# Kernel optimization log

Measured on AMD Instinct MI355X. Metric: run time of the kernel, lower is better.

The kernel has to match this reference:

```python
import jax, jax.numpy as jnp
import numpy as np

N = 131072
H = 64
CMB_RADIUS_KM = 3485.0


def setup_inputs() -> dict:
    key = jax.random.key(0)
    ks = jax.random.split(key, 8)
    phi = jax.random.uniform(ks[0], (N, 1), jnp.float32, 0.0, 2.0 * np.pi)
    # keep theta away from the poles so sin(theta) != 0
    theta = jax.random.uniform(ks[1], (N, 1), jnp.float32, 0.1, np.pi - 0.1)
    radius = jnp.full((N, 1), CMB_RADIUS_KM, dtype=jnp.float32)
    horiz_theta = jax.random.normal(ks[2], (N, 1), jnp.float32) * 0.01
    horiz_phi = jax.random.normal(ks[3], (N, 1), jnp.float32) * 0.01
    br = jax.random.normal(ks[4], (N, 1), jnp.float32) * 100.0
    W1 = jax.random.normal(ks[5], (2, H), jnp.float32) / np.sqrt(2.0)
    b1 = jnp.zeros((H,), jnp.float32)
    W2 = jax.random.normal(ks[6], (H, H), jnp.float32) / np.sqrt(H)
    b2 = jnp.zeros((H,), jnp.float32)
    W3 = jax.random.normal(ks[7], (H, 1), jnp.float32) / np.sqrt(H)
    b3 = jnp.zeros((1,), jnp.float32)
    return dict(phi=phi, theta=theta, radius=radius, horiz_theta=horiz_theta,
                horiz_phi=horiz_phi, br=br, W1=W1, b1=b1, W2=W2, b2=b2, W3=W3, b3=b3)


def reference(phi, theta, radius, horiz_theta, horiz_phi, br, W1, b1, W2, b2, W3, b3):
    sin = jnp.sin

    # per-point scalar network; input order matches torch.cat([phi, theta], dim=1)
    def T(p, t):
        x = jnp.stack([p, t])
        h = jnp.tanh(x @ W1 + b1)
        h = jnp.tanh(h @ W2 + b2)
        return (h @ W3 + b3)[0]

    dTp = jax.grad(T, 0)
    dTt = jax.grad(T, 1)

    # In the torch code T = model(X) and P = model(X) are the same function,
    # so T_x == P_x and the flows simplify to:
    def u_th(p, t):
        return dTp(p, t) / sin(t) + dTt(p, t)

    def u_ph(p, t):
        return dTp(p, t) / sin(t) - dTt(p, t)

    # nested derivatives exactly as the chained autograd.grad calls
    u_th_t = jax.grad(lambda p, t: -u_th(p, t) * sin(t), 1)            # u_theta_theta
    u_th_tt = jax.grad(lambda p, t: u_th_t(p, t) * sin(t), 1)          # u_theta_theta_theta
    u_th_p = jax.grad(lambda p, t: -u_th(p, t), 0)                     # u_theta_phi
    u_th_pp = jax.grad(u_th_p, 0)                                      # u_theta_phi_phi
    u_ph_t = jax.grad(lambda p, t: u_ph(p, t) * sin(t), 1)             # u_phi_theta
    u_ph_tt = jax.grad(lambda p, t: u_ph_t(p, t) * sin(t), 1)          # u_phi_theta_theta
    u_ph_p = jax.grad(u_ph, 0)                                         # u_phi_phi
    u_ph_pp = jax.grad(u_ph_p, 0)                                      # u_phi_phi_phi

    def per_point(p, t):
        return (u_th(p, t), u_ph(p, t), u_th_t(p, t), u_th_tt(p, t),
                u_th_pp(p, t), u_ph_tt(p, t), u_ph_p(p, t), u_ph_pp(p, t))

    vals = jax.vmap(per_point)(phi.ravel(), theta.ravel())
    ut, up, utt, uttt, utpp, uphtt, upp, uppp = [v.reshape(-1, 1) for v in vals]

    s = sin(theta)
    div_uh = (utt + upp) / (radius * s)
    u_theta_lap = s / radius ** 2 * uttt + utpp / (radius * s) ** 2
    u_phi_lap = s / radius ** 2 * uphtt + uppp / (radius * s) ** 2
    comp = s * (u_theta_lap ** 2 + u_phi_lap ** 2)
    sv_out = -(ut * horiz_theta + up * horiz_phi) - br * div_uh
    tg_con = div_uh - ut * jnp.tan(theta) / radius
    return (ut, up, div_uh, sv_out, tg_con, comp)
```

## Files before the change

kernel.cpp:

```cpp
#include <hip/hip_runtime.h>

#define NH 64

typedef _Float16 half8 __attribute__((ext_vector_type(8)));
typedef float float4v __attribute__((ext_vector_type(4)));

__device__ __forceinline__ float fast_tanh(float x) {
  float e = __expf(2.0f * x);
  float r = __builtin_amdgcn_rcpf(e + 1.0f);
  return fmaf(-2.0f, r, 1.0f);
}

__global__ __launch_bounds__(256) __attribute__((amdgpu_waves_per_eu(2, 2)))
void pinn_mfma(
    const float* __restrict__ phi, const float* __restrict__ theta,
    const float* __restrict__ radius, const float* __restrict__ hth,
    const float* __restrict__ hph, const float* __restrict__ br,
    const float* __restrict__ W1, const float* __restrict__ b1,
    const float* __restrict__ W2, const float* __restrict__ b2,
    const float* __restrict__ W3, float* __restrict__ out, int n) {
  __shared__ _Float16 Bs[2 * 4096];

  for (int i = threadIdx.x; i < 4096; i += 256) {
    int h = i >> 6, j = i & 63;
    float w2 = W2[i];
    int nt = j >> 4, cl = j & 15, ks = h >> 5, q = (h >> 3) & 3, j2 = h & 7;
    int base = (nt * 2 + ks) * 512 + (q * 16 + cl) * 8 + j2;
    _Float16 hi = (_Float16)w2;
    Bs[base] = hi;
    Bs[base + 4096] = (_Float16)(w2 - (float)hi);
  }
  __syncthreads();

  const int lane = threadIdx.x & 63;
  const int wave = threadIdx.x >> 6;
  const int tile = blockIdx.x * 4 + wave;
  const int quad = lane >> 4, col = lane & 15;
  const int pbase = tile * 16;
  if (pbase >= n) return;

  float p = phi[pbase + col], t = theta[pbase + col];
  half8 A0h[2], A0l[2], A1h[2], A1l[2], A2h[2], A2l[2];
  half8 A3[2], A4[2], A5[2], A6[2], A7[2], A8[2], A9[2];
#pragma unroll
  for (int ks = 0; ks < 2; ++ks) {
#pragma unroll
    for (int jj = 0; jj < 8; ++jj) {
      int h = ks * 32 + quad * 8 + jj;
      float a = W1[h], b = W1[NH + h];
      float z = fmaf(p, a, fmaf(t, b, b1[h]));
      float y = fast_tanh(z);
      float f1 = fmaf(-y, y, 1.0f);
      float f3 = f1 * fmaf(-6.0f, f1, 4.0f);
      float na = -2.0f * (y * f1);
      float a2 = a * a, ab = a * b, bb = b * b;
      float f3a2 = f3 * a2, f3bb = f3 * bb;
      float v1 = f1 * a, v2 = f1 * b;
      _Float16 yh = (_Float16)y;
      _Float16 v1h = (_Float16)v1;
      _Float16 v2h = (_Float16)v2;
      A0h[ks][jj] = yh;   A0l[ks][jj] = (_Float16)(y - (float)yh);
      A1h[ks][jj] = v1h;  A1l[ks][jj] = (_Float16)(v1 - (float)v1h);
      A2h[ks][jj] = v2h;  A2l[ks][jj] = (_Float16)(v2 - (float)v2h);
      A3[ks][jj] = (_Float16)(na * a2);
      A4[ks][jj] = (_Float16)(na * ab);
      A5[ks][jj] = (_Float16)(na * bb);
      A6[ks][jj] = (_Float16)(f3a2 * a);
      A7[ks][jj] = (_Float16)(f3a2 * b);
      A8[ks][jj] = (_Float16)(f3bb * a);
      A9[ks][jj] = (_Float16)(f3bb * b);
    }
  }

  const int rsel = col >> 2;
  const int pi = pbase + quad * 4 + rsel;
  float t2 = theta[pi];
  float rv = radius[pi];
  float hthv = hth[pi], hphv = hph[pi], brv = br[pi];
  float b2a[4], w3a[4];
#pragma unroll
  for (int nt = 0; nt < 4; ++nt) {
    b2a[nt] = b2[nt * 16 + col];
    w3a[nt] = W3[nt * 16 + col];
  }

  float4v Tacc[9];
#pragma unroll
  for (int x = 0; x < 9; ++x) Tacc[x] = (float4v){0.f, 0.f, 0.f, 0.f};

#pragma unroll
  for (int nt = 0; nt < 4; ++nt) {
    float4v acc[10];
#pragma unroll
    for (int k = 0; k < 10; ++k) acc[k] = (float4v){0.f, 0.f, 0.f, 0.f};
#pragma unroll
    for (int ks = 0; ks < 2; ++ks) {
      half8 bh = *(const half8*)(Bs + (nt * 2 + ks) * 512 + lane * 8);
      half8 bl = *(const half8*)(Bs + 4096 + (nt * 2 + ks) * 512 + lane * 8);
      acc[0] = __builtin_amdgcn_mfma_f32_16x16x32_f16(A0h[ks], bh, acc[0], 0, 0, 0);
      acc[0] = __builtin_amdgcn_mfma_f32_16x16x32_f16(A0l[ks], bh, acc[0], 0, 0, 0);
      acc[0] = __builtin_amdgcn_mfma_f32_16x16x32_f16(A0h[ks], bl, acc[0], 0, 0, 0);
      acc[1] = __builtin_amdgcn_mfma_f32_16x16x32_f16(A1h[ks], bh, acc[1], 0, 0, 0);
      acc[1] = __builtin_amdgcn_mfma_f32_16x16x32_f16(A1l[ks], bh, acc[1], 0, 0, 0);
      acc[1] = __builtin_amdgcn_mfma_f32_16x16x32_f16(A1h[ks], bl, acc[1], 0, 0, 0);
      acc[2] = __builtin_amdgcn_mfma_f32_16x16x32_f16(A2h[ks], bh, acc[2], 0, 0, 0);
      acc[2] = __builtin_amdgcn_mfma_f32_16x16x32_f16(A2l[ks], bh, acc[2], 0, 0, 0);
      acc[2] = __builtin_amdgcn_mfma_f32_16x16x32_f16(A2h[ks], bl, acc[2], 0, 0, 0);
      acc[3] = __builtin_amdgcn_mfma_f32_16x16x32_f16(A3[ks], bh, acc[3], 0, 0, 0);
      acc[4] = __builtin_amdgcn_mfma_f32_16x16x32_f16(A4[ks], bh, acc[4], 0, 0, 0);
      acc[5] = __builtin_amdgcn_mfma_f32_16x16x32_f16(A5[ks], bh, acc[5], 0, 0, 0);
      acc[6] = __builtin_amdgcn_mfma_f32_16x16x32_f16(A6[ks], bh, acc[6], 0, 0, 0);
      acc[7] = __builtin_amdgcn_mfma_f32_16x16x32_f16(A7[ks], bh, acc[7], 0, 0, 0);
      acc[8] = __builtin_amdgcn_mfma_f32_16x16x32_f16(A8[ks], bh, acc[8], 0, 0, 0);
      acc[9] = __builtin_amdgcn_mfma_f32_16x16x32_f16(A9[ks], bh, acc[9], 0, 0, 0);
    }
    float b2v = b2a[nt];
    float w3v = w3a[nt];
#pragma unroll
    for (int r = 0; r < 4; ++r) {
      float z0 = acc[0][r] + b2v;
      float y2 = fast_tanh(z0);
      float g1 = fmaf(-y2, y2, 1.0f);
      float g2 = -2.0f * (y2 * g1);
      float g3 = g1 * fmaf(-6.0f, g1, 4.0f);
      float gp = acc[1][r], gt = acc[2][r];
      float gpp = acc[3][r], gpt = acc[4][r], gtt = acc[5][r];
      float zppp = acc[6][r], zppt = acc[7][r], zptt = acc[8][r], zttt = acc[9][r];
      float c2p = g2 * gp, c2t = g2 * gt;
      float c2p2 = c2p + c2p, c2t2 = c2t + c2t;
      float gp2 = gp * gp, gt2 = gt * gt;
      Tacc[0][r] = fmaf(w3v, g1 * gp, Tacc[0][r]);
      Tacc[1][r] = fmaf(w3v, g1 * gt, Tacc[1][r]);
      Tacc[2][r] = fmaf(w3v, fmaf(c2p, gp, g1 * gpp), Tacc[2][r]);
      Tacc[3][r] = fmaf(w3v, fmaf(c2p, gt, g1 * gpt), Tacc[3][r]);
      Tacc[4][r] = fmaf(w3v, fmaf(c2t, gt, g1 * gtt), Tacc[4][r]);
      Tacc[5][r] = fmaf(w3v, fmaf(g3, gp2 * gp, fmaf(c2p2 + c2p, gpp, g1 * zppp)), Tacc[5][r]);
      Tacc[6][r] = fmaf(w3v, fmaf(g3, gp2 * gt, fmaf(c2p2, gpt, fmaf(c2t, gpp, g1 * zppt))), Tacc[6][r]);
      Tacc[7][r] = fmaf(w3v, fmaf(g3, gp * gt2, fmaf(c2t2, gpt, fmaf(c2p, gtt, g1 * zptt))), Tacc[7][r]);
      Tacc[8][r] = fmaf(w3v, fmaf(g3, gt2 * gt, fmaf(c2t2 + c2t, gtt, g1 * zttt)), Tacc[8][r]);
    }
  }

  float T[9];
#pragma unroll
  for (int x = 0; x < 9; ++x) {
    float4v v = Tacc[x];
    bool hi8 = (col & 8) != 0;
    float k0 = hi8 ? v[2] : v[0];
    float k1 = hi8 ? v[3] : v[1];
    float s0 = hi8 ? v[0] : v[2];
    float s1 = hi8 ? v[1] : v[3];
    float p0 = k0 + __shfl_xor(s0, 8, 16);
    float p1 = k1 + __shfl_xor(s1, 8, 16);
    bool hi4 = (col & 4) != 0;
    float kk = hi4 ? p1 : p0;
    float ss = hi4 ? p0 : p1;
    float q = kk + __shfl_xor(ss, 4, 16);
    q += __shfl_xor(q, 2, 16);
    q += __shfl_xor(q, 1, 16);
    T[x] = q;
  }
  float Tp = T[0], Tt = T[1], Tpp = T[2], Tpt = T[3], Ttt = T[4];
  float Tppp = T[5], Tppt = T[6], Tptt = T[7], Tttt = T[8];

  float rev = t2 * 0.15915494309189535f;
  float s = __builtin_amdgcn_sinf(rev);
  float c = __builtin_amdgcn_cosf(rev);
  float inv_s = __builtin_amdgcn_rcpf(s);
  float inv_s2 = inv_s * inv_s;

  float A = Tp * inv_s + Tt;
  float D = Tp * inv_s - Tt;
  float q1 = Tpt * inv_s - Tp * c * inv_s2;
  float A_t = q1 + Ttt;
  float D_t = q1 - Ttt;
  float q2 = Tptt * inv_s - 2.0f * Tpt * c * inv_s2
           + Tp * (s * s + 2.0f * c * c) * inv_s2 * inv_s;
  float A_tt = q2 + Tttt;
  float D_tt = q2 - Tttt;
  float A_pp = Tppp * inv_s + Tppt;
  float D_p  = Tpp * inv_s - Tpt;
  float D_pp = Tppp * inv_s - Tppt;

  float utt   = -(A_t * s + A * c);
  float uttt  = -(A_tt * s + 2.0f * A_t * c - A * s) * s + utt * c;
  float utpp  = -A_pp;
  float upht  = D_t * s + D * c;
  float uphtt = (D_tt * s + 2.0f * D_t * c - D * s) * s + upht * c;
  float upp   = D_p;
  float uppp  = D_pp;

  float inv_r = __builtin_amdgcn_rcpf(rv);
  float inv_r2 = inv_r * inv_r;
  float div_uh = (utt + upp) * inv_r * inv_s;
  float lap_t = s * inv_r2 * uttt + utpp * inv_s2 * inv_r2;
  float lap_p = s * inv_r2 * uphtt + uppp * inv_s2 * inv_r2;
  float comp = s * (lap_t * lap_t + lap_p * lap_p);
  float sv = -(A * hthv + D * hphv) - brv * div_uh;
  float tg = div_uh - A * s * __builtin_amdgcn_rcpf(c) * inv_r;

  if ((col & 3) == 0) {
    out[pi]         = A;
    out[n + pi]     = D;
    out[2 * n + pi] = div_uh;
    out[3 * n + pi] = sv;
    out[4 * n + pi] = tg;
    out[5 * n + pi] = comp;
  }
}

extern "C" void kernel_launch(void* const* d_in, const int* in_sizes, int n_in,
                              void* d_out, int out_size, void* d_ws, size_t ws_size,
                              hipStream_t stream) {
  const float* phi    = (const float*)d_in[0];
  const float* theta  = (const float*)d_in[1];
  const float* radius = (const float*)d_in[2];
  const float* hth    = (const float*)d_in[3];
  const float* hph    = (const float*)d_in[4];
  const float* br     = (const float*)d_in[5];
  const float* W1     = (const float*)d_in[6];
  const float* b1     = (const float*)d_in[7];
  const float* W2     = (const float*)d_in[8];
  const float* b2     = (const float*)d_in[9];
  const float* W3     = (const float*)d_in[10];
  (void)ws_size; (void)n_in; (void)out_size; (void)d_ws;

  float* out = (float*)d_out;
  int n = in_sizes[0];

  int ntiles = (n + 15) / 16;
  int nblocks = (ntiles + 3) / 4;
  pinn_mfma<<<nblocks, 256, 0, stream>>>(
      phi, theta, radius, hth, hph, br, W1, b1, W2, b2, W3, out, n);
}
```

Measured before the change: 111.8 us.

## Precompute split-fp16 W2 fragments in a prep kernel, load B from global

Moves the per-block conversion of W2 into hi/lo fp16 MFMA fragments out of the main kernel into a small prep kernel that writes them to workspace. The main kernel drops the shared-memory staging and the __syncthreads, and loads B fragments straight from global/L2. W1/b1 loads are also vectorised, and the per-point input loads are hoisted ahead of the activation math. In exchange it adds a second kernel launch and repeated global reads of B instead of LDS reads.

```diff
diff --git a/kernel.cpp b/kernel.cpp
--- a/kernel.cpp
+++ b/kernel.cpp
@@ -9,6 +9,27 @@
   float e = __expf(2.0f * x);
   float r = __builtin_amdgcn_rcpf(e + 1.0f);
   return fmaf(-2.0f, r, 1.0f);
+}
+
+__global__ void prep_B(const float* __restrict__ W2, _Float16* __restrict__ ws) {
+  int i = blockIdx.x * 256 + threadIdx.x;
+  if (i >= 2 * 4096) return;
+  int s = i >> 12;
+  int off = i & 4095;
+  int nt = off >> 10;
+  int ks = (off >> 9) & 1;
+  int ln = (off >> 3) & 63;
+  int jj = off & 7;
+  int h = ks * 32 + (ln >> 4) * 8 + jj;
+  int j = nt * 16 + (ln & 15);
+  float w2 = W2[h * NH + j];
+  _Float16 hi = (_Float16)w2;
+  ws[(s * 8 + nt * 2 + ks) * 512 + ln * 8 + jj] =
+      (s == 0) ? hi : (_Float16)(w2 - (float)hi);
+}
+
+__device__ __forceinline__ half8 ldB(const _Float16* ws, int s, int nt, int ks, int lane) {
+  return *(const half8*)(ws + (s * 8 + nt * 2 + ks) * 512 + lane * 8);
 }
 
 __global__ __launch_bounds__(256) __attribute__((amdgpu_waves_per_eu(2, 2)))
@@ -17,21 +38,8 @@
     const float* __restrict__ radius, const float* __restrict__ hth,
     const float* __restrict__ hph, const float* __restrict__ br,
     const float* __restrict__ W1, const float* __restrict__ b1,
-    const float* __restrict__ W2, const float* __restrict__ b2,
-    const float* __restrict__ W3, float* __restrict__ out, int n) {
-  __shared__ _Float16 Bs[2 * 4096];
-
-  for (int i = threadIdx.x; i < 4096; i += 256) {
-    int h = i >> 6, j = i & 63;
-    float w2 = W2[i];
-    int nt = j >> 4, cl = j & 15, ks = h >> 5, q = (h >> 3) & 3, j2 = h & 7;
-    int base = (nt * 2 + ks) * 512 + (q * 16 + cl) * 8 + j2;
-    _Float16 hi = (_Float16)w2;
-    Bs[base] = hi;
-    Bs[base + 4096] = (_Float16)(w2 - (float)hi);
-  }
-  __syncthreads();
-
+    const float* __restrict__ b2, const float* __restrict__ W3,
+    const _Float16* __restrict__ Bws, float* __restrict__ out, int n) {
   const int lane = threadIdx.x & 63;
   const int wave = threadIdx.x >> 6;
   const int tile = blockIdx.x * 4 + wave;
@@ -40,15 +48,38 @@
   if (pbase >= n) return;
 
   float p = phi[pbase + col], t = theta[pbase + col];
+
+  const float4v* W1v = (const float4v*)W1;
+  const float4v* b1v = (const float4v*)b1;
+  float4v aV[2][2], bV[2][2], cV[2][2];
+  aV[0][0] = W1v[quad * 2];      aV[0][1] = W1v[quad * 2 + 1];
+  aV[1][0] = W1v[8 + quad * 2];  aV[1][1] = W1v[8 + quad * 2 + 1];
+  bV[0][0] = W1v[16 + quad * 2]; bV[0][1] = W1v[16 + quad * 2 + 1];
+  bV[1][0] = W1v[24 + quad * 2]; bV[1][1] = W1v[24 + quad * 2 + 1];
+  cV[0][0] = b1v[quad * 2];      cV[0][1] = b1v[quad * 2 + 1];
+  cV[1][0] = b1v[8 + quad * 2];  cV[1][1] = b1v[8 + quad * 2 + 1];
+
+  const int rsel = col >> 2;
+  const int pi = pbase + quad * 4 + rsel;
+  float t2 = theta[pi];
+  float rv = radius[pi];
+  float hthv = hth[pi], hphv = hph[pi], brv = br[pi];
+  float b2a[4], w3a[4];
+#pragma unroll
+  for (int nt = 0; nt < 4; ++nt) {
+    b2a[nt] = b2[nt * 16 + col];
+    w3a[nt] = W3[nt * 16 + col];
+  }
+
   half8 A0h[2], A0l[2], A1h[2], A1l[2], A2h[2], A2l[2];
   half8 A3[2], A4[2], A5[2], A6[2], A7[2], A8[2], A9[2];
 #pragma unroll
   for (int ks = 0; ks < 2; ++ks) {
 #pragma unroll
     for (int jj = 0; jj < 8; ++jj) {
-      int h = ks * 32 + quad * 8 + jj;
-      float a = W1[h], b = W1[NH + h];
-      float z = fmaf(p, a, fmaf(t, b, b1[h]));
+      float a = aV[ks][jj >> 2][jj & 3];
+      float b = bV[ks][jj >> 2][jj & 3];
+      float z = fmaf(p, a, fmaf(t, b, cV[ks][jj >> 2][jj & 3]));
       float y = fast_tanh(z);
       float f1 = fmaf(-y, y, 1.0f);
       float f3 = f1 * fmaf(-6.0f, f1, 4.0f);
@@ -72,18 +103,6 @@
     }
   }
 
-  const int rsel = col >> 2;
-  const int pi = pbase + quad * 4 + rsel;
-  float t2 = theta[pi];
-  float rv = radius[pi];
-  float hthv = hth[pi], hphv = hph[pi], brv = br[pi];
-  float b2a[4], w3a[4];
-#pragma unroll
-  for (int nt = 0; nt < 4; ++nt) {
-    b2a[nt] = b2[nt * 16 + col];
-    w3a[nt] = W3[nt * 16 + col];
-  }
-
   float4v Tacc[9];
 #pragma unroll
   for (int x = 0; x < 9; ++x) Tacc[x] = (float4v){0.f, 0.f, 0.f, 0.f};
@@ -95,8 +114,8 @@
     for (int k = 0; k < 10; ++k) acc[k] = (float4v){0.f, 0.f, 0.f, 0.f};
 #pragma unroll
     for (int ks = 0; ks < 2; ++ks) {
-      half8 bh = *(const half8*)(Bs + (nt * 2 + ks) * 512 + lane * 8);
-      half8 bl = *(const half8*)(Bs + 4096 + (nt * 2 + ks) * 512 + lane * 8);
+      half8 bh = ldB(Bws, 0, nt, ks, lane);
+      half8 bl = ldB(Bws, 1, nt, ks, lane);
       acc[0] = __builtin_amdgcn_mfma_f32_16x16x32_f16(A0h[ks], bh, acc[0], 0, 0, 0);
       acc[0] = __builtin_amdgcn_mfma_f32_16x16x32_f16(A0l[ks], bh, acc[0], 0, 0, 0);
       acc[0] = __builtin_amdgcn_mfma_f32_16x16x32_f16(A0h[ks], bl, acc[0], 0, 0, 0);
@@ -223,13 +242,15 @@
   const float* W2     = (const float*)d_in[8];
   const float* b2     = (const float*)d_in[9];
   const float* W3     = (const float*)d_in[10];
-  (void)ws_size; (void)n_in; (void)out_size; (void)d_ws;
-
+  (void)ws_size; (void)n_in; (void)out_size;
+
+  _Float16* Bws = (_Float16*)d_ws;
   float* out = (float*)d_out;
   int n = in_sizes[0];
 
+  prep_B<<<(2 * 4096 + 255) / 256, 256, 0, stream>>>(W2, Bws);
   int ntiles = (n + 15) / 16;
   int nblocks = (ntiles + 3) / 4;
   pinn_mfma<<<nblocks, 256, 0, stream>>>(
-      phi, theta, radius, hth, hph, br, W1, b1, W2, b2, W3, out, n);
-}
+      phi, theta, radius, hth, hph, br, W1, b1, b2, W3, Bws, out, n);
+}
```

Result: faster. 109.4 us (-2.1%).
